# Optimization experiments

Hardware: AMD Instinct MI355X
Metric: run time of the kernel (lower is better)

Reference implementation:

```python
import jax, jax.numpy as jnp
from jax import lax
import numpy as np

B, T, C, H, K = 16, 1024, 1024, 16, 31
PAD = K // 2


def setup_inputs() -> dict:
    key = jax.random.key(0)
    ks = jax.random.split(key, 10)
    inp = {
        "query": jax.random.normal(ks[0], (B, T, C), jnp.float32),
        "key": jax.random.normal(ks[1], (B, T, C), jnp.float32),
        "value": jax.random.normal(ks[2], (B, T, C), jnp.float32),
        "mask": jnp.ones((B, 1, T), jnp.int32),
        # linear1: n_feat -> 2*n_feat ; linear2: 2*n_feat -> n_feat (torch Linear convention W:(out,in))
        "W1": jax.random.normal(ks[3], (2 * C, C), jnp.float32) / np.sqrt(C),
        "b1": jnp.zeros((2 * C,), jnp.float32),
        "W2": jax.random.normal(ks[4], (C, 2 * C), jnp.float32) / np.sqrt(2 * C),
        "b2": jnp.zeros((C,), jnp.float32),
        # shared depthwise kernels, uniform(0,1) as in the torch init
        "weight": jax.random.uniform(ks[5], (H, 1, K), jnp.float32),
        "weight_f": jax.random.uniform(ks[6], (1, 1, K), jnp.float32),
    }
    return inp


def reference(query, key, value, mask, W1, b1, W2, b2, weight, weight_f):
    # eval mode: dropout is identity (dropout_rate irrelevant); use_kernel_mask=False, use_bias=False
    x = query @ W1.T + b1                      # (B,T,2C)
    a, g = jnp.split(x, 2, axis=-1)
    x = a * jax.nn.sigmoid(g)                  # GLU -> (B,T,C)

    dn = ("NCH", "OIH", "NCH")
    # 2D branch: conv along the FEATURE axis with a single softmax-normalized kernel,
    # shared across all (b,t) positions (the torch code replicates weight_f B*T times).
    wf = jax.nn.softmax(weight_f, axis=-1)     # (1,1,K)
    xf = lax.conv_general_dilated(
        x.reshape(B * T, 1, C), wf, (1,), [(PAD, PAD)], dimension_numbers=dn
    ).reshape(B, T, C)

    # time branch: depthwise conv over time, kernel shared across C//H channels per head.
    # channel c uses head h = c % H (from view(-1, H, T) on contiguous (B,C,T)).
    w = jax.nn.softmax(weight, axis=-1)        # (H,1,K)
    xt = x.transpose(0, 2, 1).reshape(B * (C // H), H, T)
    xc = lax.conv_general_dilated(
        xt, w, (1,), [(PAD, PAD)], dimension_numbers=dn, feature_group_count=H
    ).reshape(B, C, T).transpose(0, 2, 1)      # (B,T,C)

    x = jnp.concatenate([xc, xf], axis=-1)     # (B,T,2C)
    m = jnp.transpose(mask, (0, 2, 1))         # (B,T,1)
    x = jnp.where(m == 0, 0.0, x)
    return x @ W2.T + b2                       # (B,T,C)
```

## Files before the change

### kernel.cpp

```cpp
#include <hip/hip_runtime.h>
#include <hip/hip_bf16.h>

#define B_  16
#define T_  1024
#define C_  1024
#define H_  16
#define KW_ 31
#define M_  (B_ * T_)
#define N1_ (2 * C_)
#define K1_ C_
#define N2_ C_
#define K2_ (2 * C_)

typedef __attribute__((ext_vector_type(8))) short bf16x8;
typedef __attribute__((ext_vector_type(4))) short s16x4;
typedef __attribute__((ext_vector_type(4))) float f32x4;

typedef const __attribute__((address_space(1))) void GV;
typedef __attribute__((address_space(3))) void LV;

__device__ __forceinline__ short f2bf(float f) {
  union { float f; unsigned u; } v; v.f = f;
  unsigned r = v.u + 0x7fffu + ((v.u >> 16) & 1u);
  return (short)(r >> 16);
}
__device__ __forceinline__ float b2f(short s) {
  union { float f; unsigned u; } v;
  v.u = ((unsigned)(unsigned short)s) << 16;
  return v.f;
}

__global__ __launch_bounds__(256) void prep_all(const float* __restrict__ q,
                                                const float* __restrict__ W1,
                                                const float* __restrict__ W2,
                                                const float* __restrict__ wtf,
                                                short* __restrict__ Abf,
                                                short* __restrict__ W1b,
                                                short* __restrict__ W2b) {
  const int bid = blockIdx.x;
  const int tid = threadIdx.x;
  if (bid < 4096) {
    int idx = bid * 256 + tid;
    int o = idx >> 10, j = idx & 1023;
    float e[KW_], mx = -1e30f, ssum = 0.f;
    #pragma unroll
    for (int k = 0; k < KW_; ++k) mx = fmaxf(mx, wtf[k]);
    #pragma unroll
    for (int k = 0; k < KW_; ++k) { e[k] = __expf(wtf[k] - mx); ssum += e[k]; }
    const float inv = 1.f / ssum;
    const float* base = W2 + (long)o * K2_ + C_;
    float s = 0.f;
    #pragma unroll
    for (int k = 0; k < KW_; ++k) {
      int c = j + 15 - k;
      if (c >= 0 && c < C_) s += e[k] * inv * base[c];
    }
    W2b[(long)o * K2_ + C_ + j] = f2bf(s);
  } else if (bid < 12288) {
    int idx = (bid - 4096) * 256 + tid;
    const float4* src = (const float4*)q + (long)idx * 2;
    float4 f0 = src[0], f1 = src[1];
    bf16x8 o = { f2bf(f0.x), f2bf(f0.y), f2bf(f0.z), f2bf(f0.w),
                 f2bf(f1.x), f2bf(f1.y), f2bf(f1.z), f2bf(f1.w) };
    *((bf16x8*)Abf + idx) = o;
  } else if (bid < 13312) {
    int idx = (bid - 12288) * 256 + tid;
    int r = idx >> 7;
    int c = (idx & 127) * 8;
    int s = (r & 1) ? (1024 + (r >> 1)) : (r >> 1);
    const float* src = W1 + (long)s * 1024 + c;
    bf16x8 o;
    #pragma unroll
    for (int i = 0; i < 8; ++i) o[i] = f2bf(src[i]);
    *(bf16x8*)(W1b + (long)r * 1024 + c) = o;
  } else {
    int idx = (bid - 13312) * 256 + tid;
    int o  = idx >> 7;
    int c8 = (idx & 127) * 8;
    const float* src = W2 + (long)o * K2_ + c8;
    bf16x8 v;
    #pragma unroll
    for (int i = 0; i < 8; ++i) v[i] = f2bf(src[i]);
    *(bf16x8*)(W2b + (long)o * K2_ + c8) = v;
  }
}

__global__ __launch_bounds__(256) void conv_t_k(const short* __restrict__ A2in,
                                                const float* __restrict__ wt,
                                                short* __restrict__ A2out) {
  const int tid = threadIdx.x;
  const int t0  = blockIdx.x * 64;
  const int c   = blockIdx.y * 256 + tid;
  const int b   = blockIdx.z;
  const int h   = c & (H_ - 1);

  float wk[KW_];
  {
    const float* src = wt + h * KW_;
    float mx = -1e30f, ssum = 0.f;
    #pragma unroll
    for (int k = 0; k < KW_; ++k) mx = fmaxf(mx, src[k]);
    #pragma unroll
    for (int k = 0; k < KW_; ++k) { wk[k] = __expf(src[k] - mx); ssum += wk[k]; }
    const float inv = 1.f / ssum;
    #pragma unroll
    for (int k = 0; k < KW_; ++k) wk[k] *= inv;
  }

  const long rowbase = ((long)b * T_) * K2_ + C_ + c;
  float win[KW_];
  #pragma unroll
  for (int k = 0; k < 30; ++k) {
    int t = t0 - 15 + k;
    win[k] = (t >= 0 && t < T_) ? b2f(A2in[rowbase + (long)t * K2_]) : 0.f;
  }
  for (int tt = 0; tt < 64; ++tt) {
    int tl = t0 + tt + 15;
    win[30] = (tl < T_) ? b2f(A2in[rowbase + (long)tl * K2_]) : 0.f;
    float s = 0.f;
    #pragma unroll
    for (int k = 0; k < KW_; ++k) s = fmaf(wk[k], win[k], s);
    A2out[((long)b * T_ + t0 + tt) * K2_ + c] = f2bf(s);
    #pragma unroll
    for (int k = 0; k < 30; ++k) win[k] = win[k + 1];
  }
}


#define ST_H(GP, GR0, BUFS, REG, KT, HH) do { \
    int d = tid * 16;                   \
    int rr_ = (HH) * 64 + (d >> 7);     \
    int scb = (d & 127) ^ ((rr_ & 7) << 4); \
    __builtin_amdgcn_global_load_lds( \
      (GV*)(GP + (long)(GR0 + rr_) * K + (KT) * 64 + (scb >> 1)), \
      (LV*)&lds[(BUFS) + (REG) + (HH) * 4096 + (d >> 1)], 16, 0, 0); \
  } while (0)
#define ST_A(BUFS, KT) do { ST_H(A,  arow0, BUFS, 0,    KT, 0); \
                            ST_H(A,  arow0, BUFS, 0,    KT, 1); } while (0)
#define ST_B(BUFS, KT) do { ST_H(Bw, brow0, BUFS, 8192, KT, 0); \
                            ST_H(Bw, brow0, BUFS, 8192, KT, 1); } while (0)

#define RD_A2(DST, BUFS, MP) do { \
    _Pragma("unroll") \
    for (int mm = 0; mm < 2; ++mm) \
      _Pragma("unroll") \
      for (int kk = 0; kk < 2; ++kk) { \
        int r = wm * 64 + ((MP) * 2 + mm) * 16 + rlane; \
        int byt = (r * 128 + kk * 64 + klb) ^ ((r & 7) << 4); \
        DST[mm * 2 + kk] = *(const bf16x8*)&lds[(BUFS) + (byt >> 1)]; \
      } \
  } while (0)

#define RD_B(DST, BUFS) do { \
    _Pragma("unroll") \
    for (int n = 0; n < 2; ++n) \
      _Pragma("unroll") \
      for (int kk = 0; kk < 2; ++kk) { \
        int r = wn * 32 + n * 16 + rlane; \
        int byt = (r * 128 + kk * 64 + klb) ^ ((r & 7) << 4); \
        DST[n * 2 + kk] = *(const bf16x8*)&lds[(BUFS) + 8192 + (byt >> 1)]; \
      } \
  } while (0)

#define MM(AV, BV, MP) do { \
    _Pragma("unroll") \
    for (int mm = 0; mm < 2; ++mm) \
      _Pragma("unroll") \
      for (int n = 0; n < 2; ++n) \
        _Pragma("unroll") \
        for (int kk = 0; kk < 2; ++kk) \
          acc[2 * (MP) + mm][n] = __builtin_amdgcn_mfma_f32_16x16x32_bf16( \
              AV[mm * 2 + kk], BV[n * 2 + kk], acc[2 * (MP) + mm][n], 0, 0, 0); \
  } while (0)

#define VMW(n_)  asm volatile("s_waitcnt vmcnt(" #n_ ")" ::: "memory")
#define WALLBAR() do { asm volatile("s_waitcnt lgkmcnt(0)" ::: "memory"); \
                       asm volatile("" ::: "memory"); __builtin_amdgcn_s_barrier(); \
                       __builtin_amdgcn_s_setprio(1); } while (0)
#define PRIO0() __builtin_amdgcn_s_setprio(0)

template<int MODE>
__global__ __launch_bounds__(512, 4) void gemm128(const short* __restrict__ A,
                                                  const short* __restrict__ Bw,
                                                  const float* __restrict__ bias,
                                                  void* __restrict__ Cout,
                                                  int K, int NBN, int ldo) {
  __shared__ short lds[32768];
  const int tid  = threadIdx.x;
  const int lane = tid & 63;
  const int wave = tid >> 6;
  const int wm = wave >> 2, wn = wave & 3;

  const int nwg = gridDim.x;
  const int wg  = (blockIdx.x & 7) * (nwg >> 3) + (blockIdx.x >> 3);
  const int bm = wg / NBN, bn = wg % NBN;
  const int arow0 = bm * 128, brow0 = bn * 128;

  const int rlane = lane & 15;
  const int klb   = (lane >> 4) * 16;

  f32x4 acc[4][2] = {};
  const int nt = K >> 6;
  const int ni = nt >> 1;

  bf16x8 aF[4], bA[4], bB[4];

  ST_A(0, 0); ST_B(0, 0);
  ST_B(16384, 1);
  VMW(2);
  asm volatile("" ::: "memory"); __builtin_amdgcn_s_barrier();

  for (int i = 0; i + 1 < ni; ++i) {
    const int kt1 = 2 * i + 1, kt2 = 2 * i + 2, kt3 = 2 * i + 3;
     RD_B(bA, 0); RD_A2(aF, 0, 0);         ST_A(16384, kt1);          WALLBAR(); MM(aF, bA, 0); PRIO0();
     RD_A2(aF, 0, 1);                      ST_B(0, kt2);     VMW(2);  WALLBAR(); MM(aF, bA, 1); PRIO0();
     RD_B(bB, 16384); RD_A2(aF, 16384, 0); ST_A(0, kt2);              WALLBAR(); MM(aF, bB, 0); PRIO0();
     RD_A2(aF, 16384, 1);                  ST_B(16384, kt3); VMW(2);  WALLBAR(); MM(aF, bB, 1); PRIO0();
  }
   RD_B(bA, 0); RD_A2(aF, 0, 0);           ST_A(16384, nt - 1);       WALLBAR(); MM(aF, bA, 0); PRIO0();
   RD_A2(aF, 0, 1);                                           VMW(0); WALLBAR(); MM(aF, bA, 1); PRIO0();
   RD_B(bB, 16384); RD_A2(aF, 16384, 0);                              WALLBAR(); MM(aF, bB, 0); PRIO0();
   RD_A2(aF, 16384, 1);
  asm volatile("s_waitcnt lgkmcnt(0)" ::: "memory");
  MM(aF, bB, 1);
  __builtin_amdgcn_s_setprio(0);

  #pragma unroll
  for (int m = 0; m < 4; ++m) {
    const int r = arow0 + wm * 64 + m * 16 + (lane >> 4) * 4;
    #pragma unroll
    for (int n = 0; n < 2; ++n) {
      const int c = brow0 + wn * 32 + n * 16 + (lane & 15);
      if (MODE == 0) {
        const float bb = bias[c];
        #pragma unroll
        for (int i = 0; i < 4; ++i)
          ((float*)Cout)[(long)(r + i) * ldo + c] = acc[m][n][i] + bb;
      } else {
        const int oc = (c & 1) ? (1024 + (c >> 1)) : (c >> 1);
        const float bb = bias[oc];
        #pragma unroll
        for (int i = 0; i < 4; ++i) {
          float v = acc[m][n][i] + bb;
          float o = __shfl_xor(v, 1);
          if (!(c & 1))
            ((short*)Cout)[(long)(r + i) * ldo + 1024 + (c >> 1)] =
                f2bf(v / (1.f + __expf(-o)));
        }
      }
    }
  }
}

extern "C" void kernel_launch(void* const* d_in, const int* in_sizes, int n_in,
                              void* d_out, int out_size, void* d_ws, size_t ws_size,
                              hipStream_t stream) {
  const float* q   = (const float*)d_in[0];
  const float* W1  = (const float*)d_in[4];
  const float* b1  = (const float*)d_in[5];
  const float* W2  = (const float*)d_in[6];
  const float* b2  = (const float*)d_in[7];
  const float* wt  = (const float*)d_in[8];
  const float* wtf = (const float*)d_in[9];

  short* Abf = (short*)d_ws;
  short* W1b = Abf + (long)M_ * K1_;
  short* W2b = W1b + (long)N1_ * K1_;
  short* A2  = W2b + (long)N2_ * K2_;

  prep_all<<<13824, 256, 0, stream>>>(q, W1, W2, wtf, Abf, W1b, W2b);

  gemm128<1><<<(M_ / 128) * (N1_ / 128), 512, 0, stream>>>(
      Abf, W1b, b1, A2, K1_, N1_ / 128, K2_);

  conv_t_k<<<dim3(T_ / 64, C_ / 256, B_), 256, 0, stream>>>(A2, wt, A2);

  gemm128<0><<<(M_ / 128) * (N2_ / 128), 512, 0, stream>>>(
      A2, W2b, b2, d_out, K2_, N2_ / 128, N2_);
}
```

Measured before the change: 210.5 us.

## Switch GEMMs to 256x128 tiles with 32x32 MFMA and triple-buffered LDS ring

The two bf16 GEMMs now use 256x128 block tiles, with each of 8 waves computing a 64x64 sub-tile through 32x32x16 MFMA instructions instead of 16x16x32. Staging moves to a three-slot LDS ring (144 KB) that prefetches two k-tiles ahead, with one barrier per k-step. The aim is higher arithmetic intensity per LDS read and per global load, and fewer barriers. In exchange, occupancy drops to 2 blocks per CU, register pressure rises, and the grid gets smaller.

```diff
diff --git a/kernel.cpp b/kernel.cpp
--- a/kernel.cpp
+++ b/kernel.cpp
@@ -14,7 +14,7 @@
 
 typedef __attribute__((ext_vector_type(8))) short bf16x8;
 typedef __attribute__((ext_vector_type(4))) short s16x4;
-typedef __attribute__((ext_vector_type(4))) float f32x4;
+typedef __attribute__((ext_vector_type(16))) float f32x16;
 
 typedef const __attribute__((address_space(1))) void GV;
 typedef __attribute__((address_space(3))) void LV;
@@ -127,50 +127,59 @@
 }
 
 
-#define ST_H(GP, GR0, BUFS, REG, KT, HH) do { \
-    int d = tid * 16;                   \
-    int rr_ = (HH) * 64 + (d >> 7);     \
-    int scb = (d & 127) ^ ((rr_ & 7) << 4); \
-    __builtin_amdgcn_global_load_lds( \
-      (GV*)(GP + (long)(GR0 + rr_) * K + (KT) * 64 + (scb >> 1)), \
-      (LV*)&lds[(BUFS) + (REG) + (HH) * 4096 + (d >> 1)], 16, 0, 0); \
-  } while (0)
-#define ST_A(BUFS, KT) do { ST_H(A,  arow0, BUFS, 0,    KT, 0); \
-                            ST_H(A,  arow0, BUFS, 0,    KT, 1); } while (0)
-#define ST_B(BUFS, KT) do { ST_H(Bw, brow0, BUFS, 8192, KT, 0); \
-                            ST_H(Bw, brow0, BUFS, 8192, KT, 1); } while (0)
-
-#define RD_A2(DST, BUFS, MP) do { \
-    _Pragma("unroll") \
-    for (int mm = 0; mm < 2; ++mm) \
+#define ST_A(SB, KT) do { \
+    _Pragma("unroll") \
+    for (int i = 0; i < 4; ++i) { \
+      int d = i * 8192 + tid * 16; \
+      int r = d >> 7; \
+      int scb = (d & 127) ^ ((r & 7) << 4); \
+      __builtin_amdgcn_global_load_lds( \
+        (GV*)(A + (long)(arow0 + r) * K + (KT) * 64 + (scb >> 1)), \
+        (LV*)&lds[(SB) + (d >> 1)], 16, 0, 0); \
+    } \
+  } while (0)
+#define ST_B(SB, KT) do { \
+    _Pragma("unroll") \
+    for (int i = 0; i < 2; ++i) { \
+      int d = i * 8192 + tid * 16; \
+      int r = d >> 7; \
+      int scb = (d & 127) ^ ((r & 7) << 4); \
+      __builtin_amdgcn_global_load_lds( \
+        (GV*)(Bw + (long)(brow0 + r) * K + (KT) * 64 + (scb >> 1)), \
+        (LV*)&lds[(SB) + 16384 + (d >> 1)], 16, 0, 0); \
+    } \
+  } while (0)
+
+#define RD_A(RB) do { \
+    _Pragma("unroll") \
+    for (int mb = 0; mb < 2; ++mb) \
       _Pragma("unroll") \
-      for (int kk = 0; kk < 2; ++kk) { \
-        int r = wm * 64 + ((MP) * 2 + mm) * 16 + rlane; \
-        int byt = (r * 128 + kk * 64 + klb) ^ ((r & 7) << 4); \
-        DST[mm * 2 + kk] = *(const bf16x8*)&lds[(BUFS) + (byt >> 1)]; \
+      for (int kc = 0; kc < 4; ++kc) { \
+        int r = wm * 64 + mb * 32 + l31; \
+        int byt = (r * 128 + kc * 32 + lhi * 16) ^ ((r & 7) << 4); \
+        aF[mb * 4 + kc] = *(const bf16x8*)&lds[(RB) + (byt >> 1)]; \
       } \
   } while (0)
-
-#define RD_B(DST, BUFS) do { \
-    _Pragma("unroll") \
-    for (int n = 0; n < 2; ++n) \
+#define RD_B(RB) do { \
+    _Pragma("unroll") \
+    for (int nb = 0; nb < 2; ++nb) \
       _Pragma("unroll") \
-      for (int kk = 0; kk < 2; ++kk) { \
-        int r = wn * 32 + n * 16 + rlane; \
-        int byt = (r * 128 + kk * 64 + klb) ^ ((r & 7) << 4); \
-        DST[n * 2 + kk] = *(const bf16x8*)&lds[(BUFS) + 8192 + (byt >> 1)]; \
+      for (int kc = 0; kc < 4; ++kc) { \
+        int r = wn * 64 + nb * 32 + l31; \
+        int byt = (r * 128 + kc * 32 + lhi * 16) ^ ((r & 7) << 4); \
+        bF[nb * 4 + kc] = *(const bf16x8*)&lds[(RB) + 16384 + (byt >> 1)]; \
       } \
   } while (0)
 
-#define MM(AV, BV, MP) do { \
-    _Pragma("unroll") \
-    for (int mm = 0; mm < 2; ++mm) \
+#define MM16() do { \
+    _Pragma("unroll") \
+    for (int mb = 0; mb < 2; ++mb) \
       _Pragma("unroll") \
-      for (int n = 0; n < 2; ++n) \
+      for (int nb = 0; nb < 2; ++nb) \
         _Pragma("unroll") \
-        for (int kk = 0; kk < 2; ++kk) \
-          acc[2 * (MP) + mm][n] = __builtin_amdgcn_mfma_f32_16x16x32_bf16( \
-              AV[mm * 2 + kk], BV[n * 2 + kk], acc[2 * (MP) + mm][n], 0, 0, 0); \
+        for (int kc = 0; kc < 4; ++kc) \
+          acc[mb][nb] = __builtin_amdgcn_mfma_f32_32x32x16_bf16( \
+              aF[mb * 4 + kc], bF[nb * 4 + kc], acc[mb][nb], 0, 0, 0); \
   } while (0)
 
 #define VMW(n_)  asm volatile("s_waitcnt vmcnt(" #n_ ")" ::: "memory")
@@ -178,73 +187,73 @@
                        asm volatile("" ::: "memory"); __builtin_amdgcn_s_barrier(); \
                        __builtin_amdgcn_s_setprio(1); } while (0)
 #define PRIO0() __builtin_amdgcn_s_setprio(0)
+#define RING_ADV(x) do { (x) += 24576; if ((x) == 73728) (x) = 0; } while (0)
 
 template<int MODE>
-__global__ __launch_bounds__(512, 4) void gemm128(const short* __restrict__ A,
+__global__ __launch_bounds__(512, 2) void gemm_hi(const short* __restrict__ A,
                                                   const short* __restrict__ Bw,
                                                   const float* __restrict__ bias,
                                                   void* __restrict__ Cout,
                                                   int K, int NBN, int ldo) {
-  __shared__ short lds[32768];
+  __shared__ short lds[73728];
   const int tid  = threadIdx.x;
   const int lane = tid & 63;
   const int wave = tid >> 6;
-  const int wm = wave >> 2, wn = wave & 3;
+  const int wm = wave >> 1, wn = wave & 1;
 
   const int nwg = gridDim.x;
   const int wg  = (blockIdx.x & 7) * (nwg >> 3) + (blockIdx.x >> 3);
   const int bm = wg / NBN, bn = wg % NBN;
-  const int arow0 = bm * 128, brow0 = bn * 128;
-
-  const int rlane = lane & 15;
-  const int klb   = (lane >> 4) * 16;
-
-  f32x4 acc[4][2] = {};
+  const int arow0 = bm * 256, brow0 = bn * 128;
+
+  const int l31 = lane & 31;
+  const int lhi = lane >> 5;
+
+  f32x16 acc[2][2] = {};
   const int nt = K >> 6;
-  const int ni = nt >> 1;
-
-  bf16x8 aF[4], bA[4], bB[4];
+
+  bf16x8 aF[8], bF[8];
 
   ST_A(0, 0); ST_B(0, 0);
-  ST_B(16384, 1);
-  VMW(2);
+  ST_A(24576, 1); ST_B(24576, 1);
+  VMW(6);
   asm volatile("" ::: "memory"); __builtin_amdgcn_s_barrier();
 
-  for (int i = 0; i + 1 < ni; ++i) {
-    const int kt1 = 2 * i + 1, kt2 = 2 * i + 2, kt3 = 2 * i + 3;
-     RD_B(bA, 0); RD_A2(aF, 0, 0);         ST_A(16384, kt1);          WALLBAR(); MM(aF, bA, 0); PRIO0();
-     RD_A2(aF, 0, 1);                      ST_B(0, kt2);     VMW(2);  WALLBAR(); MM(aF, bA, 1); PRIO0();
-     RD_B(bB, 16384); RD_A2(aF, 16384, 0); ST_A(0, kt2);              WALLBAR(); MM(aF, bB, 0); PRIO0();
-     RD_A2(aF, 16384, 1);                  ST_B(16384, kt3); VMW(2);  WALLBAR(); MM(aF, bB, 1); PRIO0();
-  }
-   RD_B(bA, 0); RD_A2(aF, 0, 0);           ST_A(16384, nt - 1);       WALLBAR(); MM(aF, bA, 0); PRIO0();
-   RD_A2(aF, 0, 1);                                           VMW(0); WALLBAR(); MM(aF, bA, 1); PRIO0();
-   RD_B(bB, 16384); RD_A2(aF, 16384, 0);                              WALLBAR(); MM(aF, bB, 0); PRIO0();
-   RD_A2(aF, 16384, 1);
+  int rb = 0, sb = 49152;
+  for (int t = 0; t + 2 < nt; ++t) {
+    RD_A(rb); RD_B(rb);
+    ST_A(sb, t + 2); ST_B(sb, t + 2);
+    VMW(6);
+    WALLBAR(); MM16(); PRIO0();
+    RING_ADV(rb); RING_ADV(sb);
+  }
+  RD_A(rb); RD_B(rb);
+  VMW(0);
+  WALLBAR(); MM16(); PRIO0();
+  RING_ADV(rb);
+  RD_A(rb); RD_B(rb);
   asm volatile("s_waitcnt lgkmcnt(0)" ::: "memory");
-  MM(aF, bB, 1);
+  __builtin_amdgcn_s_setprio(1);
+  MM16();
   __builtin_amdgcn_s_setprio(0);
 
   #pragma unroll
-  for (int m = 0; m < 4; ++m) {
-    const int r = arow0 + wm * 64 + m * 16 + (lane >> 4) * 4;
-    #pragma unroll
-    for (int n = 0; n < 2; ++n) {
-      const int c = brow0 + wn * 32 + n * 16 + (lane & 15);
-      if (MODE == 0) {
-        const float bb = bias[c];
-        #pragma unroll
-        for (int i = 0; i < 4; ++i)
-          ((float*)Cout)[(long)(r + i) * ldo + c] = acc[m][n][i] + bb;
-      } else {
-        const int oc = (c & 1) ? (1024 + (c >> 1)) : (c >> 1);
-        const float bb = bias[oc];
-        #pragma unroll
-        for (int i = 0; i < 4; ++i) {
-          float v = acc[m][n][i] + bb;
+  for (int mb = 0; mb < 2; ++mb) {
+    #pragma unroll
+    for (int nb = 0; nb < 2; ++nb) {
+      const int c = brow0 + wn * 64 + nb * 32 + l31;
+      #pragma unroll
+      for (int reg = 0; reg < 16; ++reg) {
+        const int r = arow0 + wm * 64 + mb * 32 + (reg & 3) + 8 * (reg >> 2) + 4 * lhi;
+        float v = acc[mb][nb][reg];
+        if (MODE == 0) {
+          ((float*)Cout)[(long)r * ldo + c] = v + bias[c];
+        } else {
+          const int oc = (c & 1) ? (1024 + (c >> 1)) : (c >> 1);
+          v += bias[oc];
           float o = __shfl_xor(v, 1);
           if (!(c & 1))
-            ((short*)Cout)[(long)(r + i) * ldo + 1024 + (c >> 1)] =
+            ((short*)Cout)[(long)r * ldo + 1024 + (c >> 1)] =
                 f2bf(v / (1.f + __expf(-o)));
         }
       }
@@ -270,11 +279,11 @@
 
   prep_all<<<13824, 256, 0, stream>>>(q, W1, W2, wtf, Abf, W1b, W2b);
 
-  gemm128<1><<<(M_ / 128) * (N1_ / 128), 512, 0, stream>>>(
+  gemm_hi<1><<<(M_ / 256) * (N1_ / 128), 512, 0, stream>>>(
       Abf, W1b, b1, A2, K1_, N1_ / 128, K2_);
 
   conv_t_k<<<dim3(T_ / 64, C_ / 256, B_), 256, 0, stream>>>(A2, wt, A2);
 
-  gemm128<0><<<(M_ / 128) * (N2_ / 128), 512, 0, stream>>>(
+  gemm_hi<0><<<(M_ / 256) * (N2_ / 128), 512, 0, stream>>>(
       A2, W2b, b2, d_out, K2_, N2_ / 128, N2_);
 }
```

After: 233.4 us. +10.8%, slower.
